# Kernel tuning notes

Hardware: AMD Instinct MI355X
Metric: run time of the kernel (lower is better)

## Reference

```python
import jax, jax.numpy as jnp
import numpy as np

N, E, IN, H, OUT = 100000, 1600000, 64, 64, 10
NEG_SLOPE = 0.2  # PyG GATConv default negative_slope


def _glorot(key, shape):
    fan = sum(shape) if len(shape) > 1 else shape[0]
    return jax.random.normal(key, shape, dtype=jnp.float32) * jnp.sqrt(2.0 / fan)


def setup_inputs() -> dict:
    key = jax.random.key(0)
    ks = jax.random.split(key, 16)
    x = jax.random.normal(ks[0], (N, IN), dtype=jnp.float32)
    edge_index = jax.random.randint(ks[1], (2, E), 0, N, dtype=jnp.int32)
    dims = [(IN, H), (H, H), (H, OUT)]
    params = {}
    for i, (fi, fo) in enumerate(dims, start=1):
        params[f"W{i}"] = _glorot(ks[4 * i - 2], (fi, fo))
        params[f"a{i}s"] = _glorot(ks[4 * i - 1], (fo,))
        params[f"a{i}d"] = _glorot(ks[4 * i], (fo,))
        params[f"b{i}"] = jnp.zeros((fo,), dtype=jnp.float32)
    return {"x": x, "edge_index": edge_index, **params}


def gat_conv(x, src, dst, W, a_s, a_d, b):
    """Single-head GATConv (PyG defaults): gather -> leaky_relu scores ->
    segment softmax over dst -> scatter-add aggregate."""
    n = x.shape[0]
    h = x @ W                                   # [N, Fo]
    alpha_src = h @ a_s                          # [N]
    alpha_dst = h @ a_d                          # [N]
    e = jax.nn.leaky_relu(alpha_src[src] + alpha_dst[dst], NEG_SLOPE)  # [E']
    m = jax.ops.segment_max(e, dst, num_segments=n)                    # stable softmax max
    ex = jnp.exp(e - m[dst])
    denom = jax.ops.segment_sum(ex, dst, num_segments=n)
    alpha = ex / denom[dst]                      # [E'] per-dst softmax
    out = jax.ops.segment_sum(alpha[:, None] * h[src], dst, num_segments=n)
    return out + b


def reference(x, edge_index, W1, a1s, a1d, b1, W2, a2s, a2d, b2, W3, a3s, a3d, b3):
    n = x.shape[0]
    loops = jnp.arange(n, dtype=edge_index.dtype)  # add_self_loops=True
    src = jnp.concatenate([edge_index[0], loops])
    dst = jnp.concatenate([edge_index[1], loops])
    h = jax.nn.relu(gat_conv(x, src, dst, W1, a1s, a1d, b1))
    # dropout is identity at inference (training=False)
    h = jax.nn.relu(gat_conv(h, src, dst, W2, a2s, a2d, b2))
    h = gat_conv(h, src, dst, W3, a3s, a3d, b3)
    return jax.nn.log_softmax(h, axis=1)
```

## Files before the change

kernel.cpp:

```cpp
#include <hip/hip_runtime.h>
#include <math.h>
#include <type_traits>


#define NEG_SLOPE 0.2f
#define BKT_BITS 9
#define BKT_SZ   512
#define PACK_SRC_BITS 20

typedef _Float16 h8v __attribute__((ext_vector_type(8)));
typedef _Float16 h4v __attribute__((ext_vector_type(4)));
typedef float f4v __attribute__((ext_vector_type(4)));

__global__ __launch_bounds__(256) void k_hist(const int* __restrict__ dst, int E,
                                              int nb, int* __restrict__ bcount) {
    __shared__ int h[BKT_SZ];
    for (int i = threadIdx.x; i < nb; i += 256) h[i] = 0;
    __syncthreads();
    for (int i = blockIdx.x * 256 + threadIdx.x; i < E; i += gridDim.x * 256)
        atomicAdd(&h[dst[i] >> BKT_BITS], 1);
    __syncthreads();
    for (int i = threadIdx.x; i < nb; i += 256)
        if (h[i]) atomicAdd(&bcount[i], h[i]);
}

__global__ __launch_bounds__(512) void k_bscan(const int* __restrict__ bcount, int nb,
                                               int E, int N, int* __restrict__ ebase,
                                               int* __restrict__ gcur,
                                               int* __restrict__ rowptr) {
    __shared__ int sm[BKT_SZ];
    int t = threadIdx.x;
    int v = (t < nb) ? bcount[t] : 0;
    sm[t] = v;
    __syncthreads();
    for (int o = 1; o < BKT_SZ; o <<= 1) {
        int tv = (t >= o) ? sm[t - o] : 0;
        __syncthreads();
        sm[t] += tv;
        __syncthreads();
    }
    int excl = sm[t] - v;
    if (t < nb) {
        ebase[t] = excl;
        gcur[t] = excl;
    }
    if (t == nb - 1) ebase[nb] = excl + v;
    if (t == 0) rowptr[N] = E + N;
}

__global__ __launch_bounds__(1024) void k_bscatter(const int* __restrict__ src,
                                                   const int* __restrict__ dst, int E,
                                                   int nb, int* __restrict__ gcur,
                                                   int* __restrict__ ebuf) {
    __shared__ int lc[BKT_SZ];
    __shared__ int gb[BKT_SZ];
    for (int i = threadIdx.x; i < nb; i += 1024) lc[i] = 0;
    __syncthreads();
    int base = blockIdx.x * 8192;
    int bkt[8], rnk[8], pk[8];
#pragma unroll
    for (int j = 0; j < 8; j++) {
        int i = base + j * 1024 + threadIdx.x;
        bkt[j] = -1;
        if (i < E) {
            int d = dst[i];
            int s = src[i];
            int b = d >> BKT_BITS;
            bkt[j] = b;
            rnk[j] = atomicAdd(&lc[b], 1);
            pk[j] = ((d & (BKT_SZ - 1)) << PACK_SRC_BITS) | s;
        }
    }
    __syncthreads();
    for (int b = threadIdx.x; b < nb; b += 1024)
        if (lc[b]) gb[b] = atomicAdd(&gcur[b], lc[b]);
    __syncthreads();
#pragma unroll
    for (int j = 0; j < 8; j++)
        if (bkt[j] >= 0) ebuf[gb[bkt[j]] + rnk[j]] = pk[j];
}

__global__ __launch_bounds__(512) void k_bcsr(const int* __restrict__ ebuf,
                                              const int* __restrict__ ebase, int N,
                                              int* __restrict__ rowptr,
                                              int* __restrict__ csr) {
    __shared__ int cnt[BKT_SZ];
    __shared__ int sm[BKT_SZ];
    int b = blockIdx.x;
    int t = threadIdx.x;
    int n0 = b << BKT_BITS;
    int nn = min(BKT_SZ, N - n0);
    cnt[t] = 0;
    __syncthreads();
    int e0 = ebase[b], e1 = ebase[b + 1];
    for (int i = e0 + t; i < e1; i += BKT_SZ)
        atomicAdd(&cnt[ebuf[i] >> PACK_SRC_BITS], 1);
    __syncthreads();
    int v = cnt[t] + (t < nn ? 1 : 0);
    sm[t] = v;
    __syncthreads();
    for (int o = 1; o < BKT_SZ; o <<= 1) {
        int tv = (t >= o) ? sm[t - o] : 0;
        __syncthreads();
        sm[t] += tv;
        __syncthreads();
    }
    int excl = sm[t] - v;
    int cb = e0 + n0;
    if (t < nn) {
        rowptr[n0 + t] = cb + excl;
        csr[cb + excl] = n0 + t;
    }
    cnt[t] = excl + 1;
    __syncthreads();
    for (int i = e0 + t; i < e1; i += BKT_SZ) {
        int p = ebuf[i];
        int dl = p >> PACK_SRC_BITS;
        int pos = atomicAdd(&cnt[dl], 1);
        csr[cb + pos] = p & ((1 << PACK_SRC_BITS) - 1);
    }
}

template <int FP>
__global__ __launch_bounds__(256) void k_gemm(
    const float* __restrict__ X, const float* __restrict__ W,
    const float* __restrict__ a_s, const float* __restrict__ a_d,
    int N, int Freal,
    _Float16* __restrict__ H, float* __restrict__ asb, float* __restrict__ adb) {
    constexpr int NT = FP / 16;
    int lane = threadIdx.x & 63;
    int quad = lane >> 4;
    int c16 = lane & 15;

    h8v bf[NT][2];
    float asv[NT], adv[NT];
#pragma unroll
    for (int nt = 0; nt < NT; nt++) {
        int n = nt * 16 + c16;
        bool ok = (n < Freal);
        asv[nt] = ok ? a_s[n] : 0.f;
        adv[nt] = ok ? a_d[n] : 0.f;
#pragma unroll
        for (int kt = 0; kt < 2; kt++)
#pragma unroll
            for (int j = 0; j < 8; j++) {
                int k = kt * 32 + quad * 8 + j;
                bf[nt][kt][j] = (_Float16)(ok ? W[k * Freal + n] : 0.f);
            }
    }

    int wid = (blockIdx.x * blockDim.x + threadIdx.x) >> 6;
    int nw = (gridDim.x * blockDim.x) >> 6;
    int ntile = (N + 15) >> 4;

    for (int t = wid; t < ntile; t += nw) {
        int m0 = t << 4;
        int row = m0 + c16;
        const float* xr = X + (size_t)min(row, N - 1) * 64;
        h8v af[2];
#pragma unroll
        for (int kt = 0; kt < 2; kt++) {
            f4v x0 = *(const f4v*)(xr + kt * 32 + quad * 8);
            f4v x1 = *(const f4v*)(xr + kt * 32 + quad * 8 + 4);
#pragma unroll
            for (int j = 0; j < 4; j++) {
                af[kt][j] = (_Float16)x0[j];
                af[kt][4 + j] = (_Float16)x1[j];
            }
        }
        f4v c[NT];
#pragma unroll
        for (int nt = 0; nt < NT; nt++) c[nt] = (f4v){0.f, 0.f, 0.f, 0.f};
#pragma unroll
        for (int kt = 0; kt < 2; kt++)
#pragma unroll
            for (int nt = 0; nt < NT; nt++)
                c[nt] = __builtin_amdgcn_mfma_f32_16x16x32_f16(af[kt], bf[nt][kt],
                                                               c[nt], 0, 0, 0);
#pragma unroll
        for (int reg = 0; reg < 4; reg++) {
            int r = m0 + quad * 4 + reg;
            if (r < N) {
#pragma unroll
                for (int nt = 0; nt < NT; nt++)
                    H[(size_t)r * FP + nt * 16 + c16] = (_Float16)c[nt][reg];
            }
        }
        float ps[4], pd[4];
#pragma unroll
        for (int reg = 0; reg < 4; reg++) {
            ps[reg] = 0.f;
            pd[reg] = 0.f;
#pragma unroll
            for (int nt = 0; nt < NT; nt++) {
                ps[reg] = fmaf(c[nt][reg], asv[nt], ps[reg]);
                pd[reg] = fmaf(c[nt][reg], adv[nt], pd[reg]);
            }
        }
        for (int o = 1; o < 16; o <<= 1) {
#pragma unroll
            for (int reg = 0; reg < 4; reg++) {
                ps[reg] += __shfl_xor(ps[reg], o, 64);
                pd[reg] += __shfl_xor(pd[reg], o, 64);
            }
        }
        if (c16 == 0) {
#pragma unroll
            for (int reg = 0; reg < 4; reg++) {
                int r = m0 + quad * 4 + reg;
                if (r < N) {
                    asb[r] = ps[reg];
                    adb[r] = pd[reg];
                }
            }
        }
    }
}

template <int FP>
__device__ __forceinline__ void agg_slow(
    int node, const _Float16* __restrict__ H, const float* __restrict__ asb,
    const float* __restrict__ adb, const float* __restrict__ bias,
    const int* __restrict__ rowptr, const int* __restrict__ csr,
    int N, int Freal, float* __restrict__ out, int mode, int lane) {
    if (node >= N) return;
    int start = rowptr[node];
    int end = rowptr[node + 1];
    float ad = adb[node];
    int lf = lane & (FP - 1);
    const float NEG_INF = -__builtin_inff();

    float m = NEG_INF;
    for (int base = start; base < end; base += 64) {
        int i = base + lane;
        if (i < end) {
            float t = asb[csr[i]] + ad;
            float e = (t > 0.f) ? t : NEG_SLOPE * t;
            m = fmaxf(m, e);
        }
    }
    for (int o = 32; o > 0; o >>= 1) m = fmaxf(m, __shfl_xor(m, o, 64));
    float dsum = 0.f, acc = 0.f;
    for (int base = start; base < end; base += 64) {
        int i = base + lane;
        int cnt = min(64, end - base);
        int s = 0;
        float p = 0.f;
        if (i < end) {
            s = csr[i];
            float t = asb[s] + ad;
            float e = (t > 0.f) ? t : NEG_SLOPE * t;
            p = __expf(e - m);
        }
        dsum += p;
        for (int j = 0; j < cnt; j++) {
            float pj = __shfl(p, j, 64);
            int sj = __shfl(s, j, 64);
            acc = fmaf(pj, (float)H[(size_t)sj * FP + lf], acc);
        }
    }
    for (int o = 32; o > 0; o >>= 1) dsum += __shfl_xor(dsum, o, 64);

    float b = (lf < Freal) ? bias[lf] : 0.f;
    float z = acc / dsum + b;
    if (mode == 0) {
        if (lane < FP) out[(size_t)node * FP + lane] = fmaxf(z, 0.f);
    } else {
        float zz = (lane < Freal) ? z : NEG_INF;
        float zm = zz;
        for (int o = 32; o > 0; o >>= 1) zm = fmaxf(zm, __shfl_xor(zm, o, 64));
        float ez = (lane < Freal) ? __expf(zz - zm) : 0.f;
        float es = ez;
        for (int o = 32; o > 0; o >>= 1) es += __shfl_xor(es, o, 64);
        if (lane < Freal) out[(size_t)node * Freal + lane] = zz - zm - __logf(es);
    }
}

template <int FP, int W>
__global__ __launch_bounds__(256) void k_agg(
    const _Float16* __restrict__ H, const float* __restrict__ asb,
    const float* __restrict__ adb, const float* __restrict__ bias,
    const int* __restrict__ rowptr, const int* __restrict__ csr,
    int N, int Freal, float* __restrict__ out, int mode) {
    constexpr int LPR = FP / W;
    constexpr int GRPH = 32 / LPR;
    using vecW = typename std::conditional<W == 8, h8v, h4v>::type;
    int lane = threadIdx.x & 63;
    int half = lane >> 5;
    int li = lane & 31;
    int wid = (blockIdx.x * blockDim.x + threadIdx.x) >> 6;
    int nA = 2 * wid;
    if (nA >= N) return;
    int n = nA + half;
    bool valid = (n < N);
    int start = 0, end = 0;
    float ad = 0.f;
    if (valid) {
        start = rowptr[n];
        end = rowptr[n + 1];
        ad = adb[n];
    }
    int deg = end - start;
    int degm = max(deg, __shfl_xor(deg, 32, 64));

    const float NEG_INF = -__builtin_inff();

    if (degm <= 32) {
        int g = li / LPR;
        int fl = li % LPR;
        int s = 0;
        float e = NEG_INF;
        if (li < deg) {
            s = csr[start + li];
            float t = asb[s] + ad;
            e = (t > 0.f) ? t : NEG_SLOPE * t;
        }
        float m = e;
        for (int o = 16; o > 0; o >>= 1) m = fmaxf(m, __shfl_xor(m, o, 64));
        float p = (li < deg) ? __expf(e - m) : 0.f;
        float dsum = p;
        for (int o = 16; o > 0; o >>= 1) dsum += __shfl_xor(dsum, o, 64);

        float acc[W];
#pragma unroll
        for (int c = 0; c < W; c++) acc[c] = 0.f;
#pragma unroll 2
        for (int jb = 0; jb < degm; jb += GRPH) {
            int gidx = half * 32 + jb + g;
            float pj = __shfl(p, gidx, 64);
            int sj = __shfl(s, gidx, 64);
            vecW r = ((const vecW*)(H + (size_t)sj * FP))[fl];
#pragma unroll
            for (int c = 0; c < W; c++) acc[c] = fmaf(pj, (float)r[c], acc[c]);
        }
        for (int o = LPR; o < 32; o <<= 1) {
#pragma unroll
            for (int c = 0; c < W; c++) acc[c] += __shfl_xor(acc[c], o, 64);
        }
        float inv = 1.f / dsum;
        int fbase = fl * W;

        if (mode == 0) {
            if (valid && li < LPR) {
                float z[W];
#pragma unroll
                for (int c = 0; c < W; c++)
                    z[c] = fmaxf(fmaf(acc[c], inv, bias[fbase + c]), 0.f);
                float4* op = (float4*)(out + (size_t)n * FP + fbase);
#pragma unroll
                for (int q = 0; q < W / 4; q++)
                    op[q] = make_float4(z[4 * q], z[4 * q + 1], z[4 * q + 2],
                                        z[4 * q + 3]);
            }
        } else {
            float zc[W];
#pragma unroll
            for (int c = 0; c < W; c++) {
                int f = fbase + c;
                zc[c] = (f < Freal) ? fmaf(acc[c], inv, bias[f]) : NEG_INF;
            }
            float vm = zc[0];
#pragma unroll
            for (int c = 1; c < W; c++) vm = fmaxf(vm, zc[c]);
            for (int o = 1; o < LPR; o <<= 1) vm = fmaxf(vm, __shfl_xor(vm, o, 64));
            float es = 0.f;
#pragma unroll
            for (int c = 0; c < W; c++) es += __expf(zc[c] - vm);
            for (int o = 1; o < LPR; o <<= 1) es += __shfl_xor(es, o, 64);
            float ls = __logf(es);
            if (valid && li < LPR) {
#pragma unroll
                for (int c = 0; c < W; c++) {
                    int f = fbase + c;
                    if (f < Freal) out[(size_t)n * Freal + f] = zc[c] - vm - ls;
                }
            }
        }
    } else {
        agg_slow<FP>(nA, H, asb, adb, bias, rowptr, csr, N, Freal, out, mode, lane);
        agg_slow<FP>(nA + 1, H, asb, adb, bias, rowptr, csr, N, Freal, out, mode, lane);
    }
}

extern "C" void kernel_launch(void* const* d_in, const int* in_sizes, int n_in,
                              void* d_out, int out_size, void* d_ws, size_t ws_size,
                              hipStream_t stream) {
    const float* x = (const float*)d_in[0];
    const int* ei = (const int*)d_in[1];
    const float* W1 = (const float*)d_in[2];
    const float* a1s = (const float*)d_in[3];
    const float* a1d = (const float*)d_in[4];
    const float* b1 = (const float*)d_in[5];
    const float* W2 = (const float*)d_in[6];
    const float* a2s = (const float*)d_in[7];
    const float* a2d = (const float*)d_in[8];
    const float* b2 = (const float*)d_in[9];
    const float* W3 = (const float*)d_in[10];
    const float* a3s = (const float*)d_in[11];
    const float* a3d = (const float*)d_in[12];
    const float* b3 = (const float*)d_in[13];

    const int N = in_sizes[0] / 64;
    const int E = in_sizes[1] / 2;
    const int Etot = E + N;
    const int nb = (N + BKT_SZ - 1) >> BKT_BITS;
    const int* srcv = ei;
    const int* dstv = ei + E;

    size_t off = 0;
    char* base = (char*)d_ws;
    auto carve = [&](size_t bytes) -> void* {
        void* p = base + off;
        off = (off + bytes + 255) & ~(size_t)255;
        return p;
    };
    int* bcount = (int*)carve((size_t)(nb + 1) * 4);
    int* ebase = (int*)carve((size_t)(nb + 1) * 4);
    int* gcur = (int*)carve((size_t)nb * 4);
    int* rowptr = (int*)carve((size_t)(N + 1) * 4);
    int* csr = (int*)carve((size_t)Etot * 4);
    float* asb = (float*)carve((size_t)N * 4);
    float* adb = (float*)carve((size_t)N * 4);
    _Float16* hA = (_Float16*)carve((size_t)N * 64 * 2);
    float* fB = (float*)carve((size_t)N * 64 * 4);
    _Float16* hC = (_Float16*)carve((size_t)N * 16 * 2);
    int* ebuf = (int*)hA;

    hipMemsetAsync(bcount, 0, (size_t)nb * 4, stream);
    k_hist<<<512, 256, 0, stream>>>(dstv, E, nb, bcount);
    k_bscan<<<1, BKT_SZ, 0, stream>>>(bcount, nb, E, N, ebase, gcur, rowptr);
    k_bscatter<<<(E + 8191) / 8192, 1024, 0, stream>>>(srcv, dstv, E, nb, gcur, ebuf);
    k_bcsr<<<nb, BKT_SZ, 0, stream>>>(ebuf, ebase, N, rowptr, csr);

    const int aggBlocks = (N + 7) / 8;
    const int gemmBlocks = 784;

    k_gemm<64><<<gemmBlocks, 256, 0, stream>>>(x, W1, a1s, a1d, N, 64, hA, asb, adb);
    k_agg<64, 8><<<aggBlocks, 256, 0, stream>>>(hA, asb, adb, b1, rowptr, csr, N, 64, fB, 0);
    k_gemm<64><<<gemmBlocks, 256, 0, stream>>>(fB, W2, a2s, a2d, N, 64, hA, asb, adb);
    k_agg<64, 8><<<aggBlocks, 256, 0, stream>>>(hA, asb, adb, b2, rowptr, csr, N, 64, fB, 0);
    k_gemm<16><<<gemmBlocks, 256, 0, stream>>>(fB, W3, a3s, a3d, N, 10, hC, asb, adb);
    k_agg<16, 4><<<aggBlocks, 256, 0, stream>>>(hC, asb, adb, b3, rowptr, csr, N, 10,
                                                (float*)d_out, 1);
}
```

Measured before the change: 341.9 us.

## Fuse dst histogram with first-layer GEMM into one launch and unroll aggregation

Merges the edge-destination histogram kernel and the layer-1 feature GEMM into a single launch in which the first blocks build the histogram and the remaining blocks run the MFMA GEMM, so the two independent stages overlap. Because the GEMM output buffer is now written before CSR construction, the bucket scatter buffer gets its own workspace allocation instead of aliasing that buffer. It also raises the unroll of the aggregation gather loop from 2 to 4. This saves one launch and the idle tail between the two stages, at the cost of extra workspace and more register pressure in the aggregation kernel.

```diff
diff --git a/kernel.cpp b/kernel.cpp
--- a/kernel.cpp
+++ b/kernel.cpp
@@ -11,18 +11,6 @@
 typedef _Float16 h8v __attribute__((ext_vector_type(8)));
 typedef _Float16 h4v __attribute__((ext_vector_type(4)));
 typedef float f4v __attribute__((ext_vector_type(4)));
-
-__global__ __launch_bounds__(256) void k_hist(const int* __restrict__ dst, int E,
-                                              int nb, int* __restrict__ bcount) {
-    __shared__ int h[BKT_SZ];
-    for (int i = threadIdx.x; i < nb; i += 256) h[i] = 0;
-    __syncthreads();
-    for (int i = blockIdx.x * 256 + threadIdx.x; i < E; i += gridDim.x * 256)
-        atomicAdd(&h[dst[i] >> BKT_BITS], 1);
-    __syncthreads();
-    for (int i = threadIdx.x; i < nb; i += 256)
-        if (h[i]) atomicAdd(&bcount[i], h[i]);
-}
 
 __global__ __launch_bounds__(512) void k_bscan(const int* __restrict__ bcount, int nb,
                                                int E, int N, int* __restrict__ ebase,
@@ -118,6 +106,121 @@
         int dl = p >> PACK_SRC_BITS;
         int pos = atomicAdd(&cnt[dl], 1);
         csr[cb + pos] = p & ((1 << PACK_SRC_BITS) - 1);
+    }
+}
+
+__device__ __forceinline__ void gemm64_body(
+    int bid, int nblocks, const float* __restrict__ X, const float* __restrict__ W,
+    const float* __restrict__ a_s, const float* __restrict__ a_d, int N,
+    _Float16* __restrict__ H, float* __restrict__ asb, float* __restrict__ adb) {
+    constexpr int NT = 4;
+    int lane = threadIdx.x & 63;
+    int quad = lane >> 4;
+    int c16 = lane & 15;
+
+    h8v bf[NT][2];
+    float asv[NT], adv[NT];
+#pragma unroll
+    for (int nt = 0; nt < NT; nt++) {
+        int n = nt * 16 + c16;
+        asv[nt] = a_s[n];
+        adv[nt] = a_d[n];
+#pragma unroll
+        for (int kt = 0; kt < 2; kt++)
+#pragma unroll
+            for (int j = 0; j < 8; j++) {
+                int k = kt * 32 + quad * 8 + j;
+                bf[nt][kt][j] = (_Float16)W[k * 64 + n];
+            }
+    }
+
+    int wid = (bid * 256 + (int)threadIdx.x) >> 6;
+    int nw = (nblocks * 256) >> 6;
+    int ntile = (N + 15) >> 4;
+
+    for (int t = wid; t < ntile; t += nw) {
+        int m0 = t << 4;
+        int row = m0 + c16;
+        const float* xr = X + (size_t)min(row, N - 1) * 64;
+        h8v af[2];
+#pragma unroll
+        for (int kt = 0; kt < 2; kt++) {
+            f4v x0 = *(const f4v*)(xr + kt * 32 + quad * 8);
+            f4v x1 = *(const f4v*)(xr + kt * 32 + quad * 8 + 4);
+#pragma unroll
+            for (int j = 0; j < 4; j++) {
+                af[kt][j] = (_Float16)x0[j];
+                af[kt][4 + j] = (_Float16)x1[j];
+            }
+        }
+        f4v c[NT];
+#pragma unroll
+        for (int nt = 0; nt < NT; nt++) c[nt] = (f4v){0.f, 0.f, 0.f, 0.f};
+#pragma unroll
+        for (int kt = 0; kt < 2; kt++)
+#pragma unroll
+            for (int nt = 0; nt < NT; nt++)
+                c[nt] = __builtin_amdgcn_mfma_f32_16x16x32_f16(af[kt], bf[nt][kt],
+                                                               c[nt], 0, 0, 0);
+#pragma unroll
+        for (int reg = 0; reg < 4; reg++) {
+            int r = m0 + quad * 4 + reg;
+            if (r < N) {
+#pragma unroll
+                for (int nt = 0; nt < NT; nt++)
+                    H[(size_t)r * 64 + nt * 16 + c16] = (_Float16)c[nt][reg];
+            }
+        }
+        float ps[4], pd[4];
+#pragma unroll
+        for (int reg = 0; reg < 4; reg++) {
+            ps[reg] = 0.f;
+            pd[reg] = 0.f;
+#pragma unroll
+            for (int nt = 0; nt < NT; nt++) {
+                ps[reg] = fmaf(c[nt][reg], asv[nt], ps[reg]);
+                pd[reg] = fmaf(c[nt][reg], adv[nt], pd[reg]);
+            }
+        }
+        for (int o = 1; o < 16; o <<= 1) {
+#pragma unroll
+            for (int reg = 0; reg < 4; reg++) {
+                ps[reg] += __shfl_xor(ps[reg], o, 64);
+                pd[reg] += __shfl_xor(pd[reg], o, 64);
+            }
+        }
+        if (c16 == 0) {
+#pragma unroll
+            for (int reg = 0; reg < 4; reg++) {
+                int r = m0 + quad * 4 + reg;
+                if (r < N) {
+                    asb[r] = ps[reg];
+                    adb[r] = pd[reg];
+                }
+            }
+        }
+    }
+}
+
+__global__ __launch_bounds__(256) void k_hist_gemm(
+    const int* __restrict__ dst, int E, int nb, int* __restrict__ bcount,
+    int histBlocks,
+    const float* __restrict__ X, const float* __restrict__ W,
+    const float* __restrict__ a_s, const float* __restrict__ a_d, int N,
+    _Float16* __restrict__ H, float* __restrict__ asb, float* __restrict__ adb) {
+    __shared__ int h[BKT_SZ];
+    int bid = blockIdx.x;
+    if (bid < histBlocks) {
+        for (int i = threadIdx.x; i < nb; i += 256) h[i] = 0;
+        __syncthreads();
+        for (int i = bid * 256 + threadIdx.x; i < E; i += histBlocks * 256)
+            atomicAdd(&h[dst[i] >> BKT_BITS], 1);
+        __syncthreads();
+        for (int i = threadIdx.x; i < nb; i += 256)
+            if (h[i]) atomicAdd(&bcount[i], h[i]);
+    } else {
+        gemm64_body(bid - histBlocks, (int)gridDim.x - histBlocks, X, W, a_s, a_d,
+                    N, H, asb, adb);
     }
 }
 
@@ -324,7 +427,7 @@
         float acc[W];
 #pragma unroll
         for (int c = 0; c < W; c++) acc[c] = 0.f;
-#pragma unroll 2
+#pragma unroll 4
         for (int jb = 0; jb < degm; jb += GRPH) {
             int gidx = half * 32 + jb + g;
             float pj = __shfl(p, gidx, 64);
@@ -424,18 +527,19 @@
     _Float16* hA = (_Float16*)carve((size_t)N * 64 * 2);
     float* fB = (float*)carve((size_t)N * 64 * 4);
     _Float16* hC = (_Float16*)carve((size_t)N * 16 * 2);
-    int* ebuf = (int*)hA;
+    int* ebuf = (int*)carve((size_t)E * 4);
+
+    const int aggBlocks = (N + 7) / 8;
+    const int gemmBlocks = 784;
+    const int histBlocks = 512;
 
     hipMemsetAsync(bcount, 0, (size_t)nb * 4, stream);
-    k_hist<<<512, 256, 0, stream>>>(dstv, E, nb, bcount);
+    k_hist_gemm<<<histBlocks + gemmBlocks, 256, 0, stream>>>(
+        dstv, E, nb, bcount, histBlocks, x, W1, a1s, a1d, N, hA, asb, adb);
     k_bscan<<<1, BKT_SZ, 0, stream>>>(bcount, nb, E, N, ebase, gcur, rowptr);
     k_bscatter<<<(E + 8191) / 8192, 1024, 0, stream>>>(srcv, dstv, E, nb, gcur, ebuf);
     k_bcsr<<<nb, BKT_SZ, 0, stream>>>(ebuf, ebase, N, rowptr, csr);
 
-    const int aggBlocks = (N + 7) / 8;
-    const int gemmBlocks = 784;
-
-    k_gemm<64><<<gemmBlocks, 256, 0, stream>>>(x, W1, a1s, a1d, N, 64, hA, asb, adb);
     k_agg<64, 8><<<aggBlocks, 256, 0, stream>>>(hA, asb, adb, b1, rowptr, csr, N, 64, fB, 0);
     k_gemm<64><<<gemmBlocks, 256, 0, stream>>>(fB, W2, a2s, a2d, N, 64, hA, asb, adb);
     k_agg<64, 8><<<aggBlocks, 256, 0, stream>>>(hA, asb, adb, b2, rowptr, csr, N, 64, fB, 0);
```

Result: faster. 329.5 us (-3.6%).
